# Optimization experiments

Measured on AMD Instinct MI355X. Metric: run time of the kernel, lower is better.

## Reference

```python
import jax, jax.numpy as jnp
import numpy as np


def setup_inputs() -> dict:
    key = jax.random.key(0)
    ks = jax.random.split(key, 6)
    B, S, T, E, D = 16, 128, 128, 512, 512  # batch, enc steps, dec steps, enc units, dec units
    scale = 0.05
    return {
        "enc": jax.random.normal(ks[0], (B, S, E), dtype=jnp.float32),
        "dec": jax.random.normal(ks[1], (B, T, D), dtype=jnp.float32),
        "W1": jax.random.normal(ks[2], (E, E), dtype=jnp.float32) * scale,
        "W2": jax.random.normal(ks[3], (D, E), dtype=jnp.float32) * scale,
        "b": jax.random.normal(ks[4], (1, 1, E), dtype=jnp.float32) * scale,
        "V": jax.random.normal(ks[5], (E, 1), dtype=jnp.float32) * scale,
    }


def reference(enc, dec, W1, W2, b, V):
    # Vectorized Bahdanau additive attention (the original loops over decoder
    # timesteps with keras.backend.rnn; the steps are independent so we batch them).
    W1_hs = jnp.einsum('bse,ef->bsf', enc, W1)            # [B,S,E] (computed once, not per step)
    W2_ht = jnp.einsum('btd,de->bte', dec, W2)            # [B,T,E]
    # tanh(W1.hs + W2.ht + b): broadcast to [B,T,S,E]
    scores = jnp.tanh(W1_hs[:, None, :, :] + W2_ht[:, :, None, :] + b)
    logits = jnp.einsum('btse,e->bts', scores, V[:, 0])   # [B,T,S]
    attn_weights = jax.nn.softmax(logits, axis=-1)        # softmax over encoder steps
    context_vectors = jnp.einsum('bts,bse->bte', attn_weights, enc)  # [B,T,E]
    return (context_vectors, attn_weights)
```

## Files before the change

kernel.cpp:

```cpp
#include <hip/hip_runtime.h>
#include <hip/hip_bf16.h>
#include <cstddef>


constexpr int nBt = 16, nSq = 128, nTq = 128, nEd = 512;

typedef __attribute__((ext_vector_type(4))) float f32x4;
typedef __attribute__((ext_vector_type(8))) short s16x8;

#define PRESCALE 2.8853900817779268f
#define LOG2E 1.4426950408889634f

__device__ __forceinline__ unsigned short to_bf(float f) {
    unsigned u = __builtin_bit_cast(unsigned, f);
    return (unsigned short)((u + 0x7FFFu + ((u >> 16) & 1u)) >> 16);
}
__device__ __forceinline__ float from_bf(unsigned short h) {
    unsigned u = ((unsigned)h) << 16;
    return __builtin_bit_cast(float, u);
}

__device__ __forceinline__ void pair_acc(
    float xa, float xb, float ca, float cb, float na, float nb, float& acc)
{
    const float A = fmaf(xa, ca, 1.0f);
    const float B = fmaf(xb, cb, 1.0f);
    const float r = __builtin_amdgcn_rcpf(A * B);
    float num = na * B;
    num = fmaf(nb, A, num);
    acc = fmaf(num, r, acc);
}

__global__ __launch_bounds__(256) void kPrep(
    const float* __restrict__ W1, const float* __restrict__ W2,
    unsigned short* __restrict__ WT,
    const float* __restrict__ enc, const float* __restrict__ dec,
    unsigned short* __restrict__ encT,
    unsigned short* __restrict__ Ah, unsigned short* __restrict__ Al)
{
    __shared__ float tl[32][33];
    const int r  = threadIdx.x >> 3;
    const int c4 = (threadIdx.x & 7) * 4;
    int bid = blockIdx.x;

    if (bid < 512) {
        const int z = bid >> 8;
        const int yx = bid & 255;
        const int kB = (yx >> 4) * 32;
        const int nB = (yx & 15) * 32;
        const float* W = z ? W2 : W1;
        const float4 v = *(const float4*)&W[(size_t)(kB + r) * nEd + nB + c4];
        tl[r][c4 + 0] = v.x; tl[r][c4 + 1] = v.y;
        tl[r][c4 + 2] = v.z; tl[r][c4 + 3] = v.w;
        __syncthreads();
        unsigned short hh[4], ll[4];
        #pragma unroll
        for (int i = 0; i < 4; ++i) {
            const float x = tl[c4 + i][r];
            hh[i] = to_bf(x);
            ll[i] = to_bf(x - from_bf(hh[i]));
        }
        const size_t o = ((size_t)z * nEd + nB + r) * nEd + kB + c4;
        *(ushort4*)&WT[o] = *(ushort4*)hh;
        *(ushort4*)&WT[(size_t)2 * nEd * nEd + o] = *(ushort4*)ll;
    } else if (bid < 1536) {
        bid -= 512;
        const int b = bid >> 6;
        const int r6 = bid & 63;
        const int eB = (r6 & 15) * 32;
        const int sB = (r6 >> 4) * 32;
        const float4 v = *(const float4*)&enc[((size_t)b * nSq + sB + r) * nEd + eB + c4];
        tl[r][c4 + 0] = v.x; tl[r][c4 + 1] = v.y;
        tl[r][c4 + 2] = v.z; tl[r][c4 + 3] = v.w;
        __syncthreads();
        unsigned short o[4];
        #pragma unroll
        for (int i = 0; i < 4; ++i) o[i] = to_bf(tl[c4 + i][r]);
        *(ushort4*)&encT[((size_t)b * nEd + eB + r) * nSq + sB + c4] = *(ushort4*)o;
    } else {
        const size_t g0 = ((size_t)(bid - 1536) * 256 + threadIdx.x) * 8;
        const int z = (int)(g0 >> 20);
        const size_t rem = g0 & 0xFFFFFu;
        const float* A = z ? dec : enc;
        const float4 a0 = *(const float4*)&A[rem];
        const float4 a1 = *(const float4*)&A[rem + 4];
        const float a8[8] = {a0.x, a0.y, a0.z, a0.w, a1.x, a1.y, a1.z, a1.w};
        unsigned short h[8], l[8];
        #pragma unroll
        for (int i = 0; i < 8; ++i) {
            h[i] = to_bf(a8[i]);
            l[i] = to_bf(a8[i] - from_bf(h[i]));
        }
        *(ushort4*)&Ah[g0]     = *(ushort4*)&h[0];
        *(ushort4*)&Ah[g0 + 4] = *(ushort4*)&h[4];
        *(ushort4*)&Al[g0]     = *(ushort4*)&l[0];
        *(ushort4*)&Al[g0 + 4] = *(ushort4*)&l[4];
    }
}

__global__ __launch_bounds__(256) void kMgemmC(
    const unsigned short* __restrict__ Ah, const unsigned short* __restrict__ Al,
    const unsigned short* __restrict__ WT, const float* __restrict__ bias,
    float* __restrict__ C0, float* __restrict__ C1)
{
    const int z = blockIdx.z;
    const unsigned short* __restrict__ Ahz = Ah + ((size_t)z << 20);
    const unsigned short* __restrict__ Alz = Al + ((size_t)z << 20);
    const unsigned short* __restrict__ Wh = WT + (size_t)z * nEd * nEd;
    const unsigned short* __restrict__ Wl = Wh + (size_t)2 * nEd * nEd;
    float* __restrict__ C = z ? C1 : C0;

    __shared__ unsigned short sAh[32][72];
    __shared__ unsigned short sAl[32][72];
    __shared__ unsigned short sBh[128][72];
    __shared__ unsigned short sBl[128][72];

    const int tid  = threadIdx.x;
    const int lane = tid & 63;
    const int wv   = tid >> 6;
    const int rowB = blockIdx.y * 32;
    const int colB = blockIdx.x * 128;

    const int ar = tid >> 3, ak = (tid & 3) * 8;
    const int ar8 = tid >> 3, ak8 = (tid & 7) * 8;
    const int br = tid >> 1, bc = (tid & 1) * 32;

    f32x4 acc[2][2] = {};
    const int l15 = lane & 15;
    const int kh  = lane >> 4;

    for (int k0 = 0; k0 < nEd; k0 += 64) {
        const size_t ao = (size_t)(rowB + ar8) * nEd + k0 + ak8;
        const s16x8 gah = *(const s16x8*)&Ahz[ao];
        const s16x8 gal = *(const s16x8*)&Alz[ao];
        const size_t wo = (size_t)(colB + br) * nEd + k0 + bc;
        s16x8 gh[4], gl[4];
        #pragma unroll
        for (int j = 0; j < 4; ++j) {
            gh[j] = *(const s16x8*)&Wh[wo + 8 * j];
            gl[j] = *(const s16x8*)&Wl[wo + 8 * j];
        }

        __syncthreads();
        *(s16x8*)&sAh[ar8][ak8] = gah;
        *(s16x8*)&sAl[ar8][ak8] = gal;
        #pragma unroll
        for (int j = 0; j < 4; ++j) {
            *(s16x8*)&sBh[br][bc + 8 * j] = gh[j];
            *(s16x8*)&sBl[br][bc + 8 * j] = gl[j];
        }
        __syncthreads();

        #pragma unroll
        for (int kk = 0; kk < 2; ++kk) {
            s16x8 fAh[2], fAl[2], fBh[2], fBl[2];
            #pragma unroll
            for (int mi = 0; mi < 2; ++mi) {
                fAh[mi] = *(const s16x8*)&sAh[mi * 16 + l15][kk * 32 + kh * 8];
                fAl[mi] = *(const s16x8*)&sAl[mi * 16 + l15][kk * 32 + kh * 8];
            }
            #pragma unroll
            for (int ni = 0; ni < 2; ++ni) {
                fBh[ni] = *(const s16x8*)&sBh[wv * 32 + ni * 16 + l15][kk * 32 + kh * 8];
                fBl[ni] = *(const s16x8*)&sBl[wv * 32 + ni * 16 + l15][kk * 32 + kh * 8];
            }
            #pragma unroll
            for (int mi = 0; mi < 2; ++mi)
                #pragma unroll
                for (int ni = 0; ni < 2; ++ni) {
                    f32x4 a = acc[mi][ni];
                    a = __builtin_amdgcn_mfma_f32_16x16x32_bf16(fAh[mi], fBh[ni], a, 0, 0, 0);
                    a = __builtin_amdgcn_mfma_f32_16x16x32_bf16(fAl[mi], fBh[ni], a, 0, 0, 0);
                    a = __builtin_amdgcn_mfma_f32_16x16x32_bf16(fAh[mi], fBl[ni], a, 0, 0, 0);
                    acc[mi][ni] = a;
                }
        }
    }

    #pragma unroll
    for (int ni = 0; ni < 2; ++ni) {
        const int col = colB + wv * 32 + ni * 16 + l15;
        const float bval = z ? bias[col] : 0.0f;
        #pragma unroll
        for (int mi = 0; mi < 2; ++mi) {
            #pragma unroll
            for (int r = 0; r < 4; ++r) {
                const int row = rowB + mi * 16 + kh * 4 + r;
                C[(size_t)row * nEd + col] =
                    __builtin_amdgcn_exp2f((acc[mi][ni][r] + bval) * PRESCALE);
            }
        }
    }
    (void)ak; (void)ar;
}

__global__ __launch_bounds__(256) void kMgemmB(
    const float* __restrict__ A0, const float* __restrict__ A1,
    const unsigned short* __restrict__ WT, const float* __restrict__ bias,
    float* __restrict__ C0, float* __restrict__ C1)
{
    const int z = blockIdx.z;
    const float* __restrict__ A = z ? A1 : A0;
    const unsigned short* __restrict__ Wh = WT + (size_t)z * nEd * nEd;
    const unsigned short* __restrict__ Wl = Wh + (size_t)2 * nEd * nEd;
    float* __restrict__ C = z ? C1 : C0;

    __shared__ unsigned short sAh[32][72];
    __shared__ unsigned short sAl[32][72];
    __shared__ unsigned short sBh[128][72];
    __shared__ unsigned short sBl[128][72];

    const int tid  = threadIdx.x;
    const int lane = tid & 63;
    const int wv   = tid >> 6;
    const int rowB = blockIdx.y * 32;
    const int colB = blockIdx.x * 128;

    const int ar = tid >> 3, ak = (tid & 7) * 8;
    const int br = tid >> 1, bc = (tid & 1) * 32;

    f32x4 acc[2][2] = {};
    const int l15 = lane & 15;
    const int kh  = lane >> 4;

    for (int k0 = 0; k0 < nEd; k0 += 64) {
        const float4 ga0 = *(const float4*)&A[(size_t)(rowB + ar) * nEd + k0 + ak];
        const float4 ga1 = *(const float4*)&A[(size_t)(rowB + ar) * nEd + k0 + ak + 4];
        const size_t wo = (size_t)(colB + br) * nEd + k0 + bc;
        s16x8 gh[4], gl[4];
        #pragma unroll
        for (int j = 0; j < 4; ++j) {
            gh[j] = *(const s16x8*)&Wh[wo + 8 * j];
            gl[j] = *(const s16x8*)&Wl[wo + 8 * j];
        }

        __syncthreads();
        {
            const float a8[8] = {ga0.x, ga0.y, ga0.z, ga0.w,
                                 ga1.x, ga1.y, ga1.z, ga1.w};
            unsigned short h[8], l[8];
            #pragma unroll
            for (int i = 0; i < 8; ++i) {
                h[i] = to_bf(a8[i]);
                l[i] = to_bf(a8[i] - from_bf(h[i]));
            }
            *(ushort4*)&sAh[ar][ak]     = *(ushort4*)&h[0];
            *(ushort4*)&sAh[ar][ak + 4] = *(ushort4*)&h[4];
            *(ushort4*)&sAl[ar][ak]     = *(ushort4*)&l[0];
            *(ushort4*)&sAl[ar][ak + 4] = *(ushort4*)&l[4];
        }
        #pragma unroll
        for (int j = 0; j < 4; ++j) {
            *(s16x8*)&sBh[br][bc + 8 * j] = gh[j];
            *(s16x8*)&sBl[br][bc + 8 * j] = gl[j];
        }
        __syncthreads();

        #pragma unroll
        for (int kk = 0; kk < 2; ++kk) {
            s16x8 fAh[2], fAl[2], fBh[2], fBl[2];
            #pragma unroll
            for (int mi = 0; mi < 2; ++mi) {
                fAh[mi] = *(const s16x8*)&sAh[mi * 16 + l15][kk * 32 + kh * 8];
                fAl[mi] = *(const s16x8*)&sAl[mi * 16 + l15][kk * 32 + kh * 8];
            }
            #pragma unroll
            for (int ni = 0; ni < 2; ++ni) {
                fBh[ni] = *(const s16x8*)&sBh[wv * 32 + ni * 16 + l15][kk * 32 + kh * 8];
                fBl[ni] = *(const s16x8*)&sBl[wv * 32 + ni * 16 + l15][kk * 32 + kh * 8];
            }
            #pragma unroll
            for (int mi = 0; mi < 2; ++mi)
                #pragma unroll
                for (int ni = 0; ni < 2; ++ni) {
                    f32x4 a = acc[mi][ni];
                    a = __builtin_amdgcn_mfma_f32_16x16x32_bf16(fAh[mi], fBh[ni], a, 0, 0, 0);
                    a = __builtin_amdgcn_mfma_f32_16x16x32_bf16(fAl[mi], fBh[ni], a, 0, 0, 0);
                    a = __builtin_amdgcn_mfma_f32_16x16x32_bf16(fAh[mi], fBl[ni], a, 0, 0, 0);
                    acc[mi][ni] = a;
                }
        }
    }

    #pragma unroll
    for (int ni = 0; ni < 2; ++ni) {
        const int col = colB + wv * 32 + ni * 16 + l15;
        const float bval = z ? bias[col] : 0.0f;
        #pragma unroll
        for (int mi = 0; mi < 2; ++mi) {
            #pragma unroll
            for (int r = 0; r < 4; ++r) {
                const int row = rowB + mi * 16 + kh * 4 + r;
                C[(size_t)row * nEd + col] =
                    __builtin_amdgcn_exp2f((acc[mi][ni][r] + bval) * PRESCALE);
            }
        }
    }
}

__global__ __launch_bounds__(256) void kLogSm(
    const float* __restrict__ X1e,
    const float* __restrict__ X2e,
    const float* __restrict__ V,
    float* __restrict__ attnw)
{
    const int tg = blockIdx.x, b = blockIdx.y;
    const int tid  = threadIdx.x;
    const int lane = tid & 63;
    const int w    = tid >> 6;
    const int s0 = w * 32;
    const int t0 = tg * 2;

    __shared__ float sm[2][nSq];

    const float4* vp = (const float4*)V;
    float4 n0 = vp[lane * 2], n1 = vp[lane * 2 + 1];
    n0.x *= -2.f; n0.y *= -2.f; n0.z *= -2.f; n0.w *= -2.f;
    n1.x *= -2.f; n1.y *= -2.f; n1.z *= -2.f; n1.w *= -2.f;

    float4 c0[2], c1[2];
    #pragma unroll
    for (int i = 0; i < 2; ++i) {
        const float4* xp = (const float4*)(X2e + ((size_t)b * nTq + t0 + i) * nEd);
        c0[i] = xp[lane * 2];
        c1[i] = xp[lane * 2 + 1];
    }

    const float* X1b = X1e + (size_t)b * nSq * nEd;
    float4 x0 = ((const float4*)(X1b + (size_t)s0 * nEd))[lane * 2];
    float4 x1 = ((const float4*)(X1b + (size_t)s0 * nEd))[lane * 2 + 1];

    #pragma unroll 4
    for (int si = 0; si < 32; ++si) {
        const float4 cx0 = x0, cx1 = x1;
        if (si < 31) {
            const float4* np = (const float4*)(X1b + (size_t)(s0 + si + 1) * nEd);
            x0 = np[lane * 2];
            x1 = np[lane * 2 + 1];
        }
        float a0 = 0.f, a1 = 0.f;
        pair_acc(cx0.x, cx0.y, c0[0].x, c0[0].y, n0.x, n0.y, a0);
        pair_acc(cx0.z, cx0.w, c0[0].z, c0[0].w, n0.z, n0.w, a0);
        pair_acc(cx1.x, cx1.y, c1[0].x, c1[0].y, n1.x, n1.y, a0);
        pair_acc(cx1.z, cx1.w, c1[0].z, c1[0].w, n1.z, n1.w, a0);
        pair_acc(cx0.x, cx0.y, c0[1].x, c0[1].y, n0.x, n0.y, a1);
        pair_acc(cx0.z, cx0.w, c0[1].z, c0[1].w, n0.z, n0.w, a1);
        pair_acc(cx1.x, cx1.y, c1[1].x, c1[1].y, n1.x, n1.y, a1);
        pair_acc(cx1.z, cx1.w, c1[1].z, c1[1].w, n1.z, n1.w, a1);

        const float p0 = a0 + __shfl_xor(a0, 1);
        const float p1 = a1 + __shfl_xor(a1, 1);
        float q = (lane & 1) ? p1 : p0;
        q += __shfl_xor(q, 2);
        q += __shfl_xor(q, 4);
        q += __shfl_xor(q, 8);
        q += __shfl_xor(q, 16);
        q += __shfl_xor(q, 32);
        if (lane < 2) sm[lane][s0 + si] = q;
    }
    __syncthreads();

    if (w < 2) {
        const float l0 = sm[w][lane], l1 = sm[w][lane + 64];
        float m = fmaxf(l0, l1);
        #pragma unroll
        for (int off = 32; off >= 1; off >>= 1)
            m = fmaxf(m, __shfl_xor(m, off));
        const float e0 = __builtin_amdgcn_exp2f((l0 - m) * LOG2E);
        const float e1 = __builtin_amdgcn_exp2f((l1 - m) * LOG2E);
        float sum = e0 + e1;
        #pragma unroll
        for (int off = 32; off >= 1; off >>= 1)
            sum += __shfl_xor(sum, off);
        const float inv = __builtin_amdgcn_rcpf(sum);
        float* ap = attnw + ((size_t)b * nTq + t0 + w) * nSq;
        ap[lane]      = e0 * inv;
        ap[lane + 64] = e1 * inv;
    }
}

__global__ __launch_bounds__(256) void kEncT(
    const float* __restrict__ enc, unsigned short* __restrict__ encT)
{
    const int b = blockIdx.z;
    __shared__ float tl[32][33];
    const int r  = threadIdx.x >> 3;
    const int c4 = (threadIdx.x & 7) * 4;
    const int sB = blockIdx.y * 32;
    const int eB = blockIdx.x * 32;
    const float4 v = *(const float4*)&enc[((size_t)b * nSq + sB + r) * nEd + eB + c4];
    tl[r][c4 + 0] = v.x; tl[r][c4 + 1] = v.y;
    tl[r][c4 + 2] = v.z; tl[r][c4 + 3] = v.w;
    __syncthreads();
    unsigned short o[4];
    #pragma unroll
    for (int i = 0; i < 4; ++i) o[i] = to_bf(tl[c4 + i][r]);
    *(ushort4*)&encT[((size_t)b * nEd + eB + r) * nSq + sB + c4] = *(ushort4*)o;
}

__global__ __launch_bounds__(256) void kCtxMM(
    const float* __restrict__ attnw,
    const unsigned short* __restrict__ encT,
    float* __restrict__ ctx)
{
    const int b  = blockIdx.z;
    const int tB = blockIdx.y * 32;
    const int eB = blockIdx.x * 64;

    __shared__ unsigned short sA[32][136];
    __shared__ unsigned short sB[64][136];

    const int tid  = threadIdx.x;
    const int lane = tid & 63;
    const int w    = tid >> 6;
    const int wm = (w >> 1) * 16;
    const int wn = (w & 1) * 32;
    const int l15 = lane & 15;
    const int kh  = lane >> 4;

    {
        const int r = tid >> 3, c = (tid & 7) * 16;
        const float* ap = &attnw[((size_t)b * nTq + tB + r) * nSq + c];
        unsigned short h[16];
        #pragma unroll
        for (int q = 0; q < 4; ++q) {
            const float4 v = *(const float4*)(ap + 4 * q);
            h[4 * q + 0] = to_bf(v.x); h[4 * q + 1] = to_bf(v.y);
            h[4 * q + 2] = to_bf(v.z); h[4 * q + 3] = to_bf(v.w);
        }
        *(s16x8*)&sA[r][c]     = *(s16x8*)&h[0];
        *(s16x8*)&sA[r][c + 8] = *(s16x8*)&h[8];
    }
    {
        const int r = tid >> 2, c = (tid & 3) * 32;
        const size_t o = ((size_t)b * nEd + eB + r) * nSq + c;
        *(s16x8*)&sB[r][c]      = *(const s16x8*)&encT[o];
        *(s16x8*)&sB[r][c + 8]  = *(const s16x8*)&encT[o + 8];
        *(s16x8*)&sB[r][c + 16] = *(const s16x8*)&encT[o + 16];
        *(s16x8*)&sB[r][c + 24] = *(const s16x8*)&encT[o + 24];
    }
    __syncthreads();

    f32x4 acc[2] = {};
    #pragma unroll
    for (int kk = 0; kk < 4; ++kk) {
        const s16x8 fA = *(const s16x8*)&sA[wm + l15][kk * 32 + kh * 8];
        #pragma unroll
        for (int ni = 0; ni < 2; ++ni) {
            const s16x8 fB = *(const s16x8*)&sB[wn + ni * 16 + l15][kk * 32 + kh * 8];
            acc[ni] = __builtin_amdgcn_mfma_f32_16x16x32_bf16(fA, fB, acc[ni], 0, 0, 0);
        }
    }

    #pragma unroll
    for (int ni = 0; ni < 2; ++ni) {
        const int e = eB + wn + ni * 16 + l15;
        #pragma unroll
        for (int r = 0; r < 4; ++r) {
            const int t = tB + wm + kh * 4 + r;
            ctx[((size_t)b * nTq + t) * nEd + e] = acc[ni][r];
        }
    }
}

extern "C" void kernel_launch(void* const* d_in, const int* in_sizes, int n_in,
                              void* d_out, int out_size, void* d_ws, size_t ws_size,
                              hipStream_t stream) {
    const float* enc = (const float*)d_in[0];
    const float* dec = (const float*)d_in[1];
    const float* W1  = (const float*)d_in[2];
    const float* W2  = (const float*)d_in[3];
    const float* bv  = (const float*)d_in[4];
    const float* V   = (const float*)d_in[5];

    float* ctx   = (float*)d_out;
    float* attnw = (float*)d_out + (size_t)nBt * nTq * nEd;

    unsigned short* WT = (unsigned short*)d_out;

    const size_t MB = (size_t)1024 * 1024;
    float* ws0 = (float*)d_ws;
    float* ws1 = ws0 + (size_t)nBt * nSq * nEd;

    const bool early = ws_size >= 18 * MB + 4096;
    unsigned short* encT = early ? (unsigned short*)((char*)d_ws + 8 * MB)
                                 : (unsigned short*)d_ws;

    if (early) {
        unsigned short* Ah = (unsigned short*)((char*)d_ws + 10 * MB);
        unsigned short* Al = (unsigned short*)((char*)d_ws + 14 * MB);
        kPrep<<<dim3(2560), dim3(256), 0, stream>>>(
            W1, W2, WT, enc, dec, encT, Ah, Al);
        kMgemmC<<<dim3(nEd / 128, (nBt * nSq) / 32, 2), dim3(256), 0, stream>>>(
            Ah, Al, WT, bv, ws0, ws1);
        kLogSm<<<dim3(nTq / 2, nBt), dim3(256), 0, stream>>>(ws0, ws1, V, attnw);
    } else {
        kPrep<<<dim3(512), dim3(256), 0, stream>>>(
            W1, W2, WT, enc, dec, encT, nullptr, nullptr);
        kMgemmB<<<dim3(nEd / 128, (nBt * nSq) / 32, 2), dim3(256), 0, stream>>>(
            enc, dec, WT, bv, ws0, ws1);
        kLogSm<<<dim3(nTq / 2, nBt), dim3(256), 0, stream>>>(ws0, ws1, V, attnw);
        kEncT<<<dim3(nEd / 32, nSq / 32, nBt), dim3(256), 0, stream>>>(enc, encT);
    }
    kCtxMM<<<dim3(nEd / 64, nTq / 32, nBt), dim3(256), 0, stream>>>(
        attnw, encT, ctx);
}
```

Before: 50.44 us.

## Store enc projection as bf16, fuse enc split into transpose, emit bf16 attention

The enc hi/lo bf16 split now happens inside the transpose blocks of the prep kernel, which shrinks that launch and avoids a second read of enc. The exp of the encoder projection is written as bf16, which halves the bytes the logits/softmax kernel reads in its main loop. The softmax kernel also writes a bf16 copy of the attention weights, so the context matmul loads them directly instead of converting fp32. The cost is extra precision loss on exp(W1·hs), which feeds the tanh-based logits.

```diff
diff --git a/kernel.cpp b/kernel.cpp
--- a/kernel.cpp
+++ b/kernel.cpp
@@ -31,7 +31,7 @@
     acc = fmaf(num, r, acc);
 }
 
-__global__ __launch_bounds__(256) void kPrep(
+__global__ __launch_bounds__(256) void kPrep2(
     const float* __restrict__ W1, const float* __restrict__ W2,
     unsigned short* __restrict__ WT,
     const float* __restrict__ enc, const float* __restrict__ dec,
@@ -69,7 +69,20 @@
         const int r6 = bid & 63;
         const int eB = (r6 & 15) * 32;
         const int sB = (r6 >> 4) * 32;
-        const float4 v = *(const float4*)&enc[((size_t)b * nSq + sB + r) * nEd + eB + c4];
+        const size_t srcRow = (size_t)b * nSq + sB + r;
+        const float4 v = *(const float4*)&enc[srcRow * nEd + eB + c4];
+        if (Ah != nullptr) {
+            const float a4[4] = {v.x, v.y, v.z, v.w};
+            unsigned short h[4], l[4];
+            #pragma unroll
+            for (int i = 0; i < 4; ++i) {
+                h[i] = to_bf(a4[i]);
+                l[i] = to_bf(a4[i] - from_bf(h[i]));
+            }
+            const size_t ao = srcRow * nEd + eB + c4;
+            *(ushort4*)&Ah[ao] = *(ushort4*)h;
+            *(ushort4*)&Al[ao] = *(ushort4*)l;
+        }
         tl[r][c4 + 0] = v.x; tl[r][c4 + 1] = v.y;
         tl[r][c4 + 2] = v.z; tl[r][c4 + 3] = v.w;
         __syncthreads();
@@ -79,11 +92,8 @@
         *(ushort4*)&encT[((size_t)b * nEd + eB + r) * nSq + sB + c4] = *(ushort4*)o;
     } else {
         const size_t g0 = ((size_t)(bid - 1536) * 256 + threadIdx.x) * 8;
-        const int z = (int)(g0 >> 20);
-        const size_t rem = g0 & 0xFFFFFu;
-        const float* A = z ? dec : enc;
-        const float4 a0 = *(const float4*)&A[rem];
-        const float4 a1 = *(const float4*)&A[rem + 4];
+        const float4 a0 = *(const float4*)&dec[g0];
+        const float4 a1 = *(const float4*)&dec[g0 + 4];
         const float a8[8] = {a0.x, a0.y, a0.z, a0.w, a1.x, a1.y, a1.z, a1.w};
         unsigned short h[8], l[8];
         #pragma unroll
@@ -91,24 +101,24 @@
             h[i] = to_bf(a8[i]);
             l[i] = to_bf(a8[i] - from_bf(h[i]));
         }
-        *(ushort4*)&Ah[g0]     = *(ushort4*)&h[0];
-        *(ushort4*)&Ah[g0 + 4] = *(ushort4*)&h[4];
-        *(ushort4*)&Al[g0]     = *(ushort4*)&l[0];
-        *(ushort4*)&Al[g0 + 4] = *(ushort4*)&l[4];
-    }
-}
-
-__global__ __launch_bounds__(256) void kMgemmC(
+        const size_t ao = ((size_t)1 << 20) + g0;
+        *(ushort4*)&Ah[ao]     = *(ushort4*)&h[0];
+        *(ushort4*)&Ah[ao + 4] = *(ushort4*)&h[4];
+        *(ushort4*)&Al[ao]     = *(ushort4*)&l[0];
+        *(ushort4*)&Al[ao + 4] = *(ushort4*)&l[4];
+    }
+}
+
+__global__ __launch_bounds__(256) void kMgemmC2(
     const unsigned short* __restrict__ Ah, const unsigned short* __restrict__ Al,
     const unsigned short* __restrict__ WT, const float* __restrict__ bias,
-    float* __restrict__ C0, float* __restrict__ C1)
+    unsigned short* __restrict__ X1bf, float* __restrict__ X2e)
 {
     const int z = blockIdx.z;
     const unsigned short* __restrict__ Ahz = Ah + ((size_t)z << 20);
     const unsigned short* __restrict__ Alz = Al + ((size_t)z << 20);
     const unsigned short* __restrict__ Wh = WT + (size_t)z * nEd * nEd;
     const unsigned short* __restrict__ Wl = Wh + (size_t)2 * nEd * nEd;
-    float* __restrict__ C = z ? C1 : C0;
 
     __shared__ unsigned short sAh[32][72];
     __shared__ unsigned short sAl[32][72];
@@ -121,7 +131,6 @@
     const int rowB = blockIdx.y * 32;
     const int colB = blockIdx.x * 128;
 
-    const int ar = tid >> 3, ak = (tid & 3) * 8;
     const int ar8 = tid >> 3, ak8 = (tid & 7) * 8;
     const int br = tid >> 1, bc = (tid & 1) * 32;
 
@@ -186,12 +195,158 @@
             #pragma unroll
             for (int r = 0; r < 4; ++r) {
                 const int row = rowB + mi * 16 + kh * 4 + r;
-                C[(size_t)row * nEd + col] =
-                    __builtin_amdgcn_exp2f((acc[mi][ni][r] + bval) * PRESCALE);
-            }
-        }
-    }
-    (void)ak; (void)ar;
+                const float e = __builtin_amdgcn_exp2f((acc[mi][ni][r] + bval) * PRESCALE);
+                if (z == 0)
+                    X1bf[(size_t)row * nEd + col] = to_bf(e);
+                else
+                    X2e[(size_t)row * nEd + col] = e;
+            }
+        }
+    }
+}
+
+__global__ __launch_bounds__(256) void kLogSmB(
+    const unsigned short* __restrict__ X1bf,
+    const float* __restrict__ X2e,
+    const float* __restrict__ V,
+    float* __restrict__ attnw,
+    unsigned short* __restrict__ attnbf)
+{
+    const int tg = blockIdx.x, b = blockIdx.y;
+    const int tid  = threadIdx.x;
+    const int lane = tid & 63;
+    const int w    = tid >> 6;
+    const int s0 = w * 32;
+    const int t0 = tg * 2;
+
+    __shared__ float sm[2][nSq];
+
+    const float4* vp = (const float4*)V;
+    float4 n0 = vp[lane * 2], n1 = vp[lane * 2 + 1];
+    n0.x *= -2.f; n0.y *= -2.f; n0.z *= -2.f; n0.w *= -2.f;
+    n1.x *= -2.f; n1.y *= -2.f; n1.z *= -2.f; n1.w *= -2.f;
+
+    float4 c0[2], c1[2];
+    #pragma unroll
+    for (int i = 0; i < 2; ++i) {
+        const float4* xp = (const float4*)(X2e + ((size_t)b * nTq + t0 + i) * nEd);
+        c0[i] = xp[lane * 2];
+        c1[i] = xp[lane * 2 + 1];
+    }
+
+    const unsigned short* X1b = X1bf + (size_t)b * nSq * nEd;
+    s16x8 xraw = *(const s16x8*)&X1b[(size_t)s0 * nEd + lane * 8];
+
+    #pragma unroll 4
+    for (int si = 0; si < 32; ++si) {
+        const s16x8 cur = xraw;
+        if (si < 31)
+            xraw = *(const s16x8*)&X1b[(size_t)(s0 + si + 1) * nEd + lane * 8];
+        float cx[8];
+        #pragma unroll
+        for (int i = 0; i < 8; ++i)
+            cx[i] = from_bf((unsigned short)cur[i]);
+
+        float a0 = 0.f, a1 = 0.f;
+        pair_acc(cx[0], cx[1], c0[0].x, c0[0].y, n0.x, n0.y, a0);
+        pair_acc(cx[2], cx[3], c0[0].z, c0[0].w, n0.z, n0.w, a0);
+        pair_acc(cx[4], cx[5], c1[0].x, c1[0].y, n1.x, n1.y, a0);
+        pair_acc(cx[6], cx[7], c1[0].z, c1[0].w, n1.z, n1.w, a0);
+        pair_acc(cx[0], cx[1], c0[1].x, c0[1].y, n0.x, n0.y, a1);
+        pair_acc(cx[2], cx[3], c0[1].z, c0[1].w, n0.z, n0.w, a1);
+        pair_acc(cx[4], cx[5], c1[1].x, c1[1].y, n1.x, n1.y, a1);
+        pair_acc(cx[6], cx[7], c1[1].z, c1[1].w, n1.z, n1.w, a1);
+
+        const float p0 = a0 + __shfl_xor(a0, 1);
+        const float p1 = a1 + __shfl_xor(a1, 1);
+        float q = (lane & 1) ? p1 : p0;
+        q += __shfl_xor(q, 2);
+        q += __shfl_xor(q, 4);
+        q += __shfl_xor(q, 8);
+        q += __shfl_xor(q, 16);
+        q += __shfl_xor(q, 32);
+        if (lane < 2) sm[lane][s0 + si] = q;
+    }
+    __syncthreads();
+
+    if (w < 2) {
+        const float l0 = sm[w][lane], l1 = sm[w][lane + 64];
+        float m = fmaxf(l0, l1);
+        #pragma unroll
+        for (int off = 32; off >= 1; off >>= 1)
+            m = fmaxf(m, __shfl_xor(m, off));
+        const float e0 = __builtin_amdgcn_exp2f((l0 - m) * LOG2E);
+        const float e1 = __builtin_amdgcn_exp2f((l1 - m) * LOG2E);
+        float sum = e0 + e1;
+        #pragma unroll
+        for (int off = 32; off >= 1; off >>= 1)
+            sum += __shfl_xor(sum, off);
+        const float inv = __builtin_amdgcn_rcpf(sum);
+        const float w0 = e0 * inv, w1 = e1 * inv;
+        const size_t ro = ((size_t)b * nTq + t0 + w) * nSq;
+        attnw[ro + lane]      = w0;
+        attnw[ro + lane + 64] = w1;
+        attnbf[ro + lane]      = to_bf(w0);
+        attnbf[ro + lane + 64] = to_bf(w1);
+    }
+}
+
+__global__ __launch_bounds__(256) void kCtxMMB(
+    const unsigned short* __restrict__ attnbf,
+    const unsigned short* __restrict__ encT,
+    float* __restrict__ ctx)
+{
+    const int b  = blockIdx.z;
+    const int tB = blockIdx.y * 32;
+    const int eB = blockIdx.x * 64;
+
+    __shared__ unsigned short sA[32][136];
+    __shared__ unsigned short sB[64][136];
+
+    const int tid  = threadIdx.x;
+    const int lane = tid & 63;
+    const int w    = tid >> 6;
+    const int wm = (w >> 1) * 16;
+    const int wn = (w & 1) * 32;
+    const int l15 = lane & 15;
+    const int kh  = lane >> 4;
+
+    {
+        const int r = tid >> 3, c = (tid & 7) * 16;
+        const size_t o = ((size_t)b * nTq + tB + r) * nSq + c;
+        *(s16x8*)&sA[r][c]     = *(const s16x8*)&attnbf[o];
+        *(s16x8*)&sA[r][c + 8] = *(const s16x8*)&attnbf[o + 8];
+    }
+    {
+        const int r = tid >> 2, c = (tid & 3) * 32;
+        const size_t o = ((size_t)b * nEd + eB + r) * nSq + c;
+        *(s16x8*)&sB[r][c]      = *(const s16x8*)&encT[o];
+        *(s16x8*)&sB[r][c + 8]  = *(const s16x8*)&encT[o + 8];
+        *(s16x8*)&sB[r][c + 16] = *(const s16x8*)&encT[o + 16];
+        *(s16x8*)&sB[r][c + 24] = *(const s16x8*)&encT[o + 24];
+    }
+    __syncthreads();
+
+    f32x4 acc[2] = {};
+    #pragma unroll
+    for (int kk = 0; kk < 4; ++kk) {
+        const s16x8 fA = *(const s16x8*)&sA[wm + l15][kk * 32 + kh * 8];
+        #pragma unroll
+        for (int ni = 0; ni < 2; ++ni) {
+            const s16x8 fB = *(const s16x8*)&sB[wn + ni * 16 + l15][kk * 32 + kh * 8];
+            acc[ni] = __builtin_amdgcn_mfma_f32_16x16x32_bf16(fA, fB, acc[ni], 0, 0, 0);
+        }
+    }
+
+    #pragma unroll
+    for (int ni = 0; ni < 2; ++ni) {
+        const int e = eB + wn + ni * 16 + l15;
+        #pragma unroll
+        for (int r = 0; r < 4; ++r) {
+            const int t = tB + wm + kh * 4 + r;
+            ctx[((size_t)b * nTq + t) * nEd + e] = acc[ni][r];
+        }
+    }
 }
 
 __global__ __launch_bounds__(256) void kMgemmB(
@@ -215,10 +370,8 @@
     const int wv   = tid >> 6;
     const int rowB = blockIdx.y * 32;
     const int colB = blockIdx.x * 128;
-
     const int ar = tid >> 3, ak = (tid & 7) * 8;
     const int br = tid >> 1, bc = (tid & 1) * 32;
-
     f32x4 acc[2][2] = {};
     const int l15 = lane & 15;
     const int kh  = lane >> 4;
@@ -233,7 +386,6 @@
             gh[j] = *(const s16x8*)&Wh[wo + 8 * j];
             gl[j] = *(const s16x8*)&Wl[wo + 8 * j];
         }
-
         __syncthreads();
         {
             const float a8[8] = {ga0.x, ga0.y, ga0.z, ga0.w,
@@ -255,7 +407,6 @@
             *(s16x8*)&sBl[br][bc + 8 * j] = gl[j];
         }
         __syncthreads();
-
         #pragma unroll
         for (int kk = 0; kk < 2; ++kk) {
             s16x8 fAh[2], fAl[2], fBh[2], fBl[2];
@@ -281,7 +432,6 @@
                 }
         }
     }
-
     #pragma unroll
     for (int ni = 0; ni < 2; ++ni) {
         const int col = colB + wv * 32 + ni * 16 + l15;
@@ -298,11 +448,9 @@
     }
 }
 
-__global__ __launch_bounds__(256) void kLogSm(
-    const float* __restrict__ X1e,
-    const float* __restrict__ X2e,
-    const float* __restrict__ V,
-    float* __restrict__ attnw)
+__global__ __launch_bounds__(256) void kLogSmF(
+    const float* __restrict__ X1e, const float* __restrict__ X2e,
+    const float* __restrict__ V, float* __restrict__ attnw)
 {
     const int tg = blockIdx.x, b = blockIdx.y;
     const int tid  = threadIdx.x;
@@ -310,14 +458,12 @@
     const int w    = tid >> 6;
     const int s0 = w * 32;
     const int t0 = tg * 2;
-
     __shared__ float sm[2][nSq];
 
     const float4* vp = (const float4*)V;
     float4 n0 = vp[lane * 2], n1 = vp[lane * 2 + 1];
     n0.x *= -2.f; n0.y *= -2.f; n0.z *= -2.f; n0.w *= -2.f;
     n1.x *= -2.f; n1.y *= -2.f; n1.z *= -2.f; n1.w *= -2.f;
-
     float4 c0[2], c1[2];
     #pragma unroll
     for (int i = 0; i < 2; ++i) {
@@ -325,11 +471,9 @@
         c0[i] = xp[lane * 2];
         c1[i] = xp[lane * 2 + 1];
     }
-
     const float* X1b = X1e + (size_t)b * nSq * nEd;
     float4 x0 = ((const float4*)(X1b + (size_t)s0 * nEd))[lane * 2];
     float4 x1 = ((const float4*)(X1b + (size_t)s0 * nEd))[lane * 2 + 1];
-
     #pragma unroll 4
     for (int si = 0; si < 32; ++si) {
         const float4 cx0 = x0, cx1 = x1;
@@ -347,7 +491,6 @@
         pair_acc(cx0.z, cx0.w, c0[1].z, c0[1].w, n0.z, n0.w, a1);
         pair_acc(cx1.x, cx1.y, c1[1].x, c1[1].y, n1.x, n1.y, a1);
         pair_acc(cx1.z, cx1.w, c1[1].z, c1[1].w, n1.z, n1.w, a1);
-
         const float p0 = a0 + __shfl_xor(a0, 1);
         const float p1 = a1 + __shfl_xor(a1, 1);
         float q = (lane & 1) ? p1 : p0;
@@ -359,7 +502,6 @@
         if (lane < 2) sm[lane][s0 + si] = q;
     }
     __syncthreads();
-
     if (w < 2) {
         const float l0 = sm[w][lane], l1 = sm[w][lane + 64];
         float m = fmaxf(l0, l1);
@@ -398,18 +540,15 @@
     *(ushort4*)&encT[((size_t)b * nEd + eB + r) * nSq + sB + c4] = *(ushort4*)o;
 }
 
-__global__ __launch_bounds__(256) void kCtxMM(
-    const float* __restrict__ attnw,
-    const unsigned short* __restrict__ encT,
+__global__ __launch_bounds__(256) void kCtxMMF(
+    const float* __restrict__ attnw, const unsigned short* __restrict__ encT,
     float* __restrict__ ctx)
 {
     const int b  = blockIdx.z;
     const int tB = blockIdx.y * 32;
     const int eB = blockIdx.x * 64;
-
     __shared__ unsigned short sA[32][136];
     __shared__ unsigned short sB[64][136];
-
     const int tid  = threadIdx.x;
     const int lane = tid & 63;
     const int w    = tid >> 6;
@@ -417,7 +556,6 @@
     const int wn = (w & 1) * 32;
     const int l15 = lane & 15;
     const int kh  = lane >> 4;
-
     {
         const int r = tid >> 3, c = (tid & 7) * 16;
         const float* ap = &attnw[((size_t)b * nTq + tB + r) * nSq + c];
@@ -440,7 +578,6 @@
         *(s16x8*)&sB[r][c + 24] = *(const s16x8*)&encT[o + 24];
     }
     __syncthreads();
-
     f32x4 acc[2] = {};
     #pragma unroll
     for (int kk = 0; kk < 4; ++kk) {
@@ -451,7 +588,6 @@
             acc[ni] = __builtin_amdgcn_mfma_f32_16x16x32_bf16(fA, fB, acc[ni], 0, 0, 0);
         }
     }
-
     #pragma unroll
     for (int ni = 0; ni < 2; ++ni) {
         const int e = eB + wn + ni * 16 + l15;
@@ -479,29 +615,36 @@
     unsigned short* WT = (unsigned short*)d_out;
 
     const size_t MB = (size_t)1024 * 1024;
-    float* ws0 = (float*)d_ws;
-    float* ws1 = ws0 + (size_t)nBt * nSq * nEd;
-
     const bool early = ws_size >= 18 * MB + 4096;
-    unsigned short* encT = early ? (unsigned short*)((char*)d_ws + 8 * MB)
-                                 : (unsigned short*)d_ws;
 
     if (early) {
-        unsigned short* Ah = (unsigned short*)((char*)d_ws + 10 * MB);
-        unsigned short* Al = (unsigned short*)((char*)d_ws + 14 * MB);
-        kPrep<<<dim3(2560), dim3(256), 0, stream>>>(
+        unsigned short* X1bf   = (unsigned short*)d_ws;
+        unsigned short* attnbf = (unsigned short*)((char*)d_ws + 2*MB);
+        float*          X2e    = (float*)((char*)d_ws + 4 * MB);
+        unsigned short* encT   = (unsigned short*)((char*)d_ws + 8*MB);
+        unsigned short* Ah     = (unsigned short*)((char*)d_ws + 10*MB);
+        unsigned short* Al     = (unsigned short*)((char*)d_ws + 14*MB);
+
+        kPrep2<<<dim3(2048), dim3(256), 0, stream>>>(
             W1, W2, WT, enc, dec, encT, Ah, Al);
-        kMgemmC<<<dim3(nEd / 128, (nBt * nSq) / 32, 2), dim3(256), 0, stream>>>(
-            Ah, Al, WT, bv, ws0, ws1);
-        kLogSm<<<dim3(nTq / 2, nBt), dim3(256), 0, stream>>>(ws0, ws1, V, attnw);
+        kMgemmC2<<<dim3(nEd / 128, (nBt * nSq) / 32, 2), dim3(256), 0, stream>>>(
+            Ah, Al, WT, bv, X1bf, X2e);
+        kLogSmB<<<dim3(nTq / 2, nBt), dim3(256), 0, stream>>>(
+            X1bf, X2e, V, attnw, attnbf);
+        kCtxMMB<<<dim3(nEd / 64, nTq / 32, nBt), dim3(256), 0, stream>>>(
+            attnbf, encT, ctx);
     } else {
-        kPrep<<<dim3(512), dim3(256), 0, stream>>>(
-            W1, W2, WT, enc, dec, encT, nullptr, nullptr);
+        float* ws0 = (float*)d_ws;
+        float* ws1 = ws0 + (size_t)nBt * nSq * nEd;
+        unsigned short* encT = (unsigned short*)d_ws;
+
+        kPrep2<<<dim3(512), dim3(256), 0, stream>>>(
+            W1, W2, WT, enc, dec, nullptr, nullptr, nullptr);
         kMgemmB<<<dim3(nEd / 128, (nBt * nSq) / 32, 2), dim3(256), 0, stream>>>(
             enc, dec, WT, bv, ws0, ws1);
-        kLogSm<<<dim3(nTq / 2, nBt), dim3(256), 0, stream>>>(ws0, ws1, V, attnw);
+        kLogSmF<<<dim3(nTq / 2, nBt), dim3(256), 0, stream>>>(ws0, ws1, V, attnw);
         kEncT<<<dim3(nEd / 32, nSq / 32, nBt), dim3(256), 0, stream>>>(enc, encT);
-    }
-    kCtxMM<<<dim3(nEd / 64, nTq / 32, nBt), dim3(256), 0, stream>>>(
-        attnw, encT, ctx);
-}
+        kCtxMMF<<<dim3(nEd / 64, nTq / 32, nBt), dim3(256), 0, stream>>>(
+            attnw, encT, ctx);
+    }
+}
```

Result: slower. 51.96 us (+3.0%).
